# Kernel tuning notes

Measured on AMD Instinct MI355X. Metric: run time of the kernel, lower is better.

## Reference

```python
import jax, jax.numpy as jnp
import numpy as np

N_NODES = 50000
N_EDGES = 800000
D_IN = 128
D_OUT = 128


def setup_inputs() -> dict:
    key = jax.random.key(0)
    k1, k2, k3, k4 = jax.random.split(key, 4)
    node_features = jax.random.normal(k1, (N_NODES, D_IN), dtype=jnp.float32)
    edge_index = jax.random.randint(k2, (2, N_EDGES), 0, N_NODES, dtype=jnp.int64)
    # nn.Linear params: weight [out, in], bias [out]
    W = jax.random.normal(k3, (D_OUT, D_IN), dtype=jnp.float32) / np.sqrt(D_IN)
    b = jax.random.normal(k4, (D_OUT,), dtype=jnp.float32) * 0.01
    return {"node_features": node_features, "edge_index": edge_index, "W": W, "b": b}


def reference(node_features, edge_index, W, b):
    source_nodes = edge_index[0]
    dest_nodes = edge_index[1]
    # gather neighbor features [E, D_in], scatter-add into [N, D_in]
    neighbor_features = node_features[source_nodes]
    aggregated = jax.ops.segment_sum(neighbor_features, dest_nodes,
                                     num_segments=node_features.shape[0])
    # nn.Linear: x @ W.T + b
    return aggregated @ W.T + b
```

## Files before the change

kernel.cpp:

```cpp
#include <hip/hip_runtime.h>


constexpr int NN = 50000;
constexpr int NE = 800000;
constexpr int D  = 128;

constexpr int BS   = 128;
constexpr int NB   = (NN + BS - 1) / BS;
constexpr int EPB  = 4096;
constexpr int NSB  = (NE + EPB - 1) / EPB;
constexpr int CAP  = 4096;

constexpr int AROWU = 136;

typedef __attribute__((ext_vector_type(8))) short bf16x8;
typedef __attribute__((ext_vector_type(4))) float f32x4;

__device__ inline unsigned short f2bf(float f) {
    unsigned u = __float_as_uint(f);
    return (unsigned short)((u + 0x7fffu + ((u >> 16) & 1u)) >> 16);
}
__device__ inline float bflo(unsigned v) { return __uint_as_float(v << 16); }
__device__ inline float bfhi(unsigned v) { return __uint_as_float(v & 0xffff0000u); }

constexpr int NF4 = NN * D / 4;
constexpr int W4  = D * D / 4;
constexpr int NBLK_P = (NF4 + W4 + 511) / 512;
constexpr int GRID_A = NSB + NBLK_P;

__global__ __launch_bounds__(512) void k_prep_bucket(
    const float* __restrict__ nf, const float* __restrict__ W,
    const int* __restrict__ ei,
    ushort* __restrict__ nfh, ushort* __restrict__ Wh,
    ushort* __restrict__ offs, unsigned* __restrict__ buf)
{
    __shared__ int hist[NB], off[NB], cur[NB];
    __shared__ unsigned spk[EPB];
    const int t = threadIdx.x;

    if (blockIdx.x < NSB) {
        const int blk = blockIdx.x;
        const int e0  = blk * EPB;
        int cnt = NE - e0; if (cnt > EPB) cnt = EPB;

        for (int i = t; i < NB; i += 512) hist[i] = 0;
        __syncthreads();

        unsigned pk[8];
        #pragma unroll
        for (int j = 0; j < 8; ++j) {
            int idx = j * 512 + t;
            if (idx < cnt) {
                int e = e0 + idx;
                unsigned s = (unsigned)ei[e];
                unsigned d = (unsigned)ei[NE + e];
                pk[j] = (d << 16) | s;
                atomicAdd(&hist[pk[j] >> 23], 1);
            }
        }
        __syncthreads();
        if (t < NB) off[t] = hist[t];
        __syncthreads();
        for (int o = 1; o < NB; o <<= 1) {
            int v = (t >= o && t < NB) ? off[t - o] : 0;
            __syncthreads();
            if (t < NB) off[t] += v;
            __syncthreads();
        }
        if (t < NB) {
            int ex = off[t] - hist[t];
            cur[t] = ex;
            offs[blk * (NB + 1) + t] = (ushort)ex;
        }
        if (t == 0) offs[blk * (NB + 1) + NB] = (ushort)cnt;
        __syncthreads();
        #pragma unroll
        for (int j = 0; j < 8; ++j) {
            int idx = j * 512 + t;
            if (idx < cnt) {
                int l = atomicAdd(&cur[pk[j] >> 23], 1);
                spk[l] = pk[j];
            }
        }
        __syncthreads();
        for (int i = t; i < cnt; i += 512)
            buf[(size_t)blk * EPB + i] = spk[i];
    } else {
        int i = (blockIdx.x - NSB) * 512 + t;
        if (i < NF4) {
            float4 v = ((const float4*)nf)[i];
            ((ushort4*)nfh)[i] = make_ushort4(f2bf(v.x), f2bf(v.y), f2bf(v.z), f2bf(v.w));
        } else if (i < NF4 + W4) {
            int k = i - NF4;
            float4 v = ((const float4*)W)[k];
            ((ushort4*)Wh)[k] = make_ushort4(f2bf(v.x), f2bf(v.y), f2bf(v.z), f2bf(v.w));
        }
    }
}

__global__ __launch_bounds__(1024, 8) void k_sort_agg(
    const unsigned* __restrict__ nfh, const unsigned* __restrict__ buf,
    const ushort* __restrict__ offs, const ushort* __restrict__ Wh,
    const float* __restrict__ bias, float* __restrict__ out)
{
    __shared__ unsigned pkbuf[CAP];
    __shared__ ushort srt[CAP];
    __shared__ int scnt[256];
    __shared__ int sbase[NSB], rbase[NSB];
    __shared__ int hist[BS], off[BS], cur[BS];
    __shared__ __align__(16) unsigned tile[BS * AROWU / 2];
    const int b = blockIdx.x, t = threadIdx.x;
    const int lane = t & 63, w = t >> 6;

    int my = 0;
    if (t < NSB) {
        int o0 = (int)offs[t * (NB + 1) + b];
        int o1 = (int)offs[t * (NB + 1) + b + 1];
        rbase[t] = o0;
        my = o1 - o0;
    }
    if (t < 256) scnt[t] = (t < NSB) ? my : 0;
    if (t < BS) hist[t] = 0;
    __syncthreads();
    for (int o = 1; o < 256; o <<= 1) {
        int v = (t >= o && t < 256) ? scnt[t - o] : 0;
        __syncthreads();
        if (t < 256) scnt[t] += v;
        __syncthreads();
    }
    if (t < NSB) sbase[t] = scnt[t] - my;
    __syncthreads();
    int total = scnt[NSB - 1];
    if (total > CAP) total = CAP;

    for (int p = t; p < total; p += 1024) {
        int lo = 0, hi = NSB - 1;
        while (lo < hi) {
            int mid = (lo + hi) >> 1;
            if (scnt[mid] > p) hi = mid; else lo = mid + 1;
        }
        unsigned pk = buf[(size_t)lo * EPB + rbase[lo] + (p - sbase[lo])];
        pkbuf[p] = pk;
        atomicAdd(&hist[(pk >> 16) & (BS - 1)], 1);
    }
    __syncthreads();

    if (t < BS) off[t] = hist[t];
    __syncthreads();
    for (int o = 1; o < BS; o <<= 1) {
        int v = (t >= o && t < BS) ? off[t - o] : 0;
        __syncthreads();
        if (t < BS) off[t] += v;
        __syncthreads();
    }
    if (t < BS) { int ex = off[t] - hist[t]; off[t] = ex; cur[t] = ex; }
    __syncthreads();
    for (int e = t; e < total; e += 1024) {
        unsigned pk = pkbuf[e];
        int n = (pk >> 16) & (BS - 1);
        int p = atomicAdd(&cur[n], 1);
        srt[p] = (ushort)(pk & 0xffffu);
    }
    __syncthreads();

    const int qq = lane >> 4;
    const int sl = lane & 15;
    const uint4* nfv = (const uint4*)nfh;

    #pragma unroll 1
    for (int i = 0; i < 8; ++i) {
        const int n = w * 8 + i;
        const int beg = off[n], e = beg + hist[n];
        float accA[8] = {0,0,0,0,0,0,0,0};
        float accB[8] = {0,0,0,0,0,0,0,0};
        for (int p = beg; p < e; p += 16) {
            const int lim = e - 1;
            uint4 v[4];
            #pragma unroll
            for (int j = 0; j < 4; ++j) {
                int pos = p + 4 * j + qq;
                bool ok = pos <= lim;
                if (!ok) pos = lim;
                int s = srt[pos];
                uint4 val = nfv[(size_t)s * 16 + sl];
                v[j].x = ok ? val.x : 0u;
                v[j].y = ok ? val.y : 0u;
                v[j].z = ok ? val.z : 0u;
                v[j].w = ok ? val.w : 0u;
            }
            #pragma unroll
            for (int j = 0; j < 4; ++j) {
                float* A = (j & 1) ? accB : accA;
                A[0] += bflo(v[j].x); A[1] += bfhi(v[j].x);
                A[2] += bflo(v[j].y); A[3] += bfhi(v[j].y);
                A[4] += bflo(v[j].z); A[5] += bfhi(v[j].z);
                A[6] += bflo(v[j].w); A[7] += bfhi(v[j].w);
            }
        }
        float r[8];
        #pragma unroll
        for (int k = 0; k < 8; ++k) {
            float x = accA[k] + accB[k];
            x += __shfl_xor(x, 16);
            x += __shfl_xor(x, 32);
            r[k] = x;
        }
        if (qq == 0) {
            uint4 o;
            o.x = (unsigned)f2bf(r[0]) | ((unsigned)f2bf(r[1]) << 16);
            o.y = (unsigned)f2bf(r[2]) | ((unsigned)f2bf(r[3]) << 16);
            o.z = (unsigned)f2bf(r[4]) | ((unsigned)f2bf(r[5]) << 16);
            o.w = (unsigned)f2bf(r[6]) | ((unsigned)f2bf(r[7]) << 16);
            *(uint4*)(tile + n * (AROWU / 2) + sl * 4) = o;
        }
    }
    __syncthreads();

    const int m = lane & 15, q = lane >> 4;
    const ushort* lds = (const ushort*)tile;
    #pragma unroll
    for (int i = 0; i < 4; ++i) {
        const int task = w + 16 * i;
        const int t16  = task >> 3;
        const int c0   = (task & 7) * 16;
        const int grow0 = b * BS + t16 * 16;
        if (grow0 < NN) {
            bf16x8 a[4];
            const ushort* arow = lds + (t16 * 16 + m) * AROWU + q * 8;
            #pragma unroll
            for (int kk = 0; kk < 4; ++kk)
                a[kk] = *(const bf16x8*)(arow + kk * 32);
            float bv = bias[c0 + m];
            f32x4 acc = { bv, bv, bv, bv };
            const ushort* wrow = Wh + (size_t)(c0 + m) * D + q * 8;
            #pragma unroll
            for (int kk = 0; kk < 4; ++kk) {
                bf16x8 bb = *(const bf16x8*)(wrow + kk * 32);
                acc = __builtin_amdgcn_mfma_f32_16x16x32_bf16(a[kk], bb, acc, 0, 0, 0);
            }
            float* op = out + (size_t)(grow0 + q * 4) * D + c0 + m;
            op[0]     = acc[0];
            op[D]     = acc[1];
            op[2 * D] = acc[2];
            op[3 * D] = acc[3];
        }
    }
}

extern "C" void kernel_launch(void* const* d_in, const int* in_sizes, int n_in,
                              void* d_out, int out_size, void* d_ws, size_t ws_size,
                              hipStream_t stream) {
    const float* nf = (const float*)d_in[0];
    const int*   ei = (const int*)d_in[1];
    const float* W  = (const float*)d_in[2];
    const float* b  = (const float*)d_in[3];
    float* out = (float*)d_out;

    ushort*   nfh  = (ushort*)d_ws;
    ushort*   Wh   = nfh + (size_t)NN * D;
    unsigned* buf  = (unsigned*)(Wh + D * D);
    ushort*   offs = (ushort*)(buf + (size_t)NSB * EPB);

    k_prep_bucket<<<GRID_A, 512, 0, stream>>>(nf, W, ei, nfh, Wh, offs, buf);
    k_sort_agg   <<<NB, 1024, 0, stream>>>((const unsigned*)nfh, buf, offs, Wh, b, out);
}
```

Baseline: 133.6 us.

## Use wavefront scans, transpose offsets layout, and per-quarter-wave node aggregation

Replaces the barrier-heavy LDS Hillis-Steele prefix scans in both kernels with wavefront shuffle scans plus a small cross-wave fixup, which removes many __syncthreads. Stores the bucket offsets transposed so the aggregation kernel reads them coalesced. Keeps gathered edge keys in registers instead of an LDS staging buffer. The gather loop now gives each 16-lane quarter-wave its own destination node, which drops the cross-lane shuffle reduction but makes per-node work imbalanced across lanes in a wave.

```diff
diff --git a/kernel.cpp b/kernel.cpp
--- a/kernel.cpp
+++ b/kernel.cpp
@@ -15,6 +15,7 @@
 
 typedef __attribute__((ext_vector_type(8))) short bf16x8;
 typedef __attribute__((ext_vector_type(4))) float f32x4;
+typedef __attribute__((ext_vector_type(2))) float f32x2;
 
 __device__ inline unsigned short f2bf(float f) {
     unsigned u = __float_as_uint(f);
@@ -22,6 +23,22 @@
 }
 __device__ inline float bflo(unsigned v) { return __uint_as_float(v << 16); }
 __device__ inline float bfhi(unsigned v) { return __uint_as_float(v & 0xffff0000u); }
+
+__device__ inline int wscan(int v) {
+    #pragma unroll
+    for (int o = 1; o < 64; o <<= 1) {
+        int u = __shfl_up(v, o);
+        if ((int)(threadIdx.x & 63) >= o) v += u;
+    }
+    return v;
+}
+
+__device__ inline void acc8(f32x2& a0, f32x2& a1, f32x2& a2, f32x2& a3, uint4 v) {
+    a0 += (f32x2){bflo(v.x), bfhi(v.x)};
+    a1 += (f32x2){bflo(v.y), bfhi(v.y)};
+    a2 += (f32x2){bflo(v.z), bfhi(v.z)};
+    a3 += (f32x2){bflo(v.w), bfhi(v.w)};
+}
 
 constexpr int NF4 = NN * D / 4;
 constexpr int W4  = D * D / 4;
@@ -34,9 +51,10 @@
     ushort* __restrict__ nfh, ushort* __restrict__ Wh,
     ushort* __restrict__ offs, unsigned* __restrict__ buf)
 {
-    __shared__ int hist[NB], off[NB], cur[NB];
+    __shared__ int hist[NB], cur[NB];
+    __shared__ int wsum[8];
     __shared__ unsigned spk[EPB];
-    const int t = threadIdx.x;
+    const int t = threadIdx.x, lane = t & 63, w = t >> 6;
 
     if (blockIdx.x < NSB) {
         const int blk = blockIdx.x;
@@ -59,20 +77,20 @@
             }
         }
         __syncthreads();
-        if (t < NB) off[t] = hist[t];
-        __syncthreads();
-        for (int o = 1; o < NB; o <<= 1) {
-            int v = (t >= o && t < NB) ? off[t - o] : 0;
-            __syncthreads();
-            if (t < NB) off[t] += v;
-            __syncthreads();
-        }
+        int h = (t < NB) ? hist[t] : 0;
+        int v = wscan(h);
+        if (lane == 63) wsum[w] = v;
+        __syncthreads();
+        int addv = 0;
+        #pragma unroll
+        for (int i = 0; i < 8; ++i) addv += (i < w) ? wsum[i] : 0;
+        v += addv;
         if (t < NB) {
-            int ex = off[t] - hist[t];
+            int ex = v - h;
             cur[t] = ex;
-            offs[blk * (NB + 1) + t] = (ushort)ex;
-        }
-        if (t == 0) offs[blk * (NB + 1) + NB] = (ushort)cnt;
+            offs[t * NSB + blk] = (ushort)ex;
+        }
+        if (t == 0) offs[NB * NSB + blk] = (ushort)cnt;
         __syncthreads();
         #pragma unroll
         for (int j = 0; j < 8; ++j) {
@@ -103,63 +121,80 @@
     const ushort* __restrict__ offs, const ushort* __restrict__ Wh,
     const float* __restrict__ bias, float* __restrict__ out)
 {
-    __shared__ unsigned pkbuf[CAP];
     __shared__ ushort srt[CAP];
     __shared__ int scnt[256];
     __shared__ int sbase[NSB], rbase[NSB];
     __shared__ int hist[BS], off[BS], cur[BS];
+    __shared__ int wred[16];
     __shared__ __align__(16) unsigned tile[BS * AROWU / 2];
     const int b = blockIdx.x, t = threadIdx.x;
     const int lane = t & 63, w = t >> 6;
 
     int my = 0;
     if (t < NSB) {
-        int o0 = (int)offs[t * (NB + 1) + b];
-        int o1 = (int)offs[t * (NB + 1) + b + 1];
+        int o0 = (int)offs[b * NSB + t];
+        int o1 = (int)offs[(b + 1) * NSB + t];
         rbase[t] = o0;
         my = o1 - o0;
     }
-    if (t < 256) scnt[t] = (t < NSB) ? my : 0;
     if (t < BS) hist[t] = 0;
-    __syncthreads();
-    for (int o = 1; o < 256; o <<= 1) {
-        int v = (t >= o && t < 256) ? scnt[t - o] : 0;
-        __syncthreads();
-        if (t < 256) scnt[t] += v;
-        __syncthreads();
-    }
-    if (t < NSB) sbase[t] = scnt[t] - my;
+    int vs = 0;
+    if (w < 4) {
+        vs = wscan(my);
+        if (lane == 63) wred[w] = vs;
+    }
+    __syncthreads();
+    if (w < 4) {
+        int addv = 0;
+        #pragma unroll
+        for (int i = 0; i < 3; ++i) addv += (i < w) ? wred[i] : 0;
+        vs += addv;
+        scnt[t] = vs;
+        if (t < NSB) sbase[t] = vs - my;
+    }
     __syncthreads();
     int total = scnt[NSB - 1];
     if (total > CAP) total = CAP;
 
-    for (int p = t; p < total; p += 1024) {
-        int lo = 0, hi = NSB - 1;
-        while (lo < hi) {
-            int mid = (lo + hi) >> 1;
-            if (scnt[mid] > p) hi = mid; else lo = mid + 1;
-        }
-        unsigned pk = buf[(size_t)lo * EPB + rbase[lo] + (p - sbase[lo])];
-        pkbuf[p] = pk;
-        atomicAdd(&hist[(pk >> 16) & (BS - 1)], 1);
-    }
-    __syncthreads();
-
-    if (t < BS) off[t] = hist[t];
-    __syncthreads();
-    for (int o = 1; o < BS; o <<= 1) {
-        int v = (t >= o && t < BS) ? off[t - o] : 0;
-        __syncthreads();
-        if (t < BS) off[t] += v;
-        __syncthreads();
-    }
-    if (t < BS) { int ex = off[t] - hist[t]; off[t] = ex; cur[t] = ex; }
-    __syncthreads();
-    for (int e = t; e < total; e += 1024) {
-        unsigned pk = pkbuf[e];
-        int n = (pk >> 16) & (BS - 1);
-        int p = atomicAdd(&cur[n], 1);
-        srt[p] = (ushort)(pk & 0xffffu);
+    unsigned mypk[4];
+    int mycnt = 0;
+    #pragma unroll
+    for (int j = 0; j < 4; ++j) {
+        int p = t + j * 1024;
+        if (p < total) {
+            int lo = 0, hi = NSB - 1;
+            while (lo < hi) {
+                int mid = (lo + hi) >> 1;
+                if (scnt[mid] > p) hi = mid; else lo = mid + 1;
+            }
+            unsigned pk = buf[(size_t)lo * EPB + rbase[lo] + (p - sbase[lo])];
+            mypk[j] = pk;
+            atomicAdd(&hist[(pk >> 16) & (BS - 1)], 1);
+            mycnt = j + 1;
+        }
+    }
+    __syncthreads();
+
+    int hv = (t < BS) ? hist[t] : 0;
+    int nv = 0;
+    if (w < 2) {
+        nv = wscan(hv);
+        if (lane == 63) wred[8 + w] = nv;
+    }
+    __syncthreads();
+    if (t < BS) {
+        int ex = nv + ((w == 1) ? wred[8] : 0) - hv;
+        off[t] = ex; cur[t] = ex;
+    }
+    __syncthreads();
+    #pragma unroll
+    for (int j = 0; j < 4; ++j) {
+        if (j < mycnt) {
+            unsigned pk = mypk[j];
+            int n = (pk >> 16) & (BS - 1);
+            int p = atomicAdd(&cur[n], 1);
+            srt[p] = (ushort)(pk & 0xffffu);
+        }
     }
     __syncthreads();
 
@@ -168,51 +203,30 @@
     const uint4* nfv = (const uint4*)nfh;
 
     #pragma unroll 1
-    for (int i = 0; i < 8; ++i) {
-        const int n = w * 8 + i;
-        const int beg = off[n], e = beg + hist[n];
-        float accA[8] = {0,0,0,0,0,0,0,0};
-        float accB[8] = {0,0,0,0,0,0,0,0};
-        for (int p = beg; p < e; p += 16) {
-            const int lim = e - 1;
-            uint4 v[4];
-            #pragma unroll
-            for (int j = 0; j < 4; ++j) {
-                int pos = p + 4 * j + qq;
-                bool ok = pos <= lim;
-                if (!ok) pos = lim;
-                int s = srt[pos];
-                uint4 val = nfv[(size_t)s * 16 + sl];
-                v[j].x = ok ? val.x : 0u;
-                v[j].y = ok ? val.y : 0u;
-                v[j].z = ok ? val.z : 0u;
-                v[j].w = ok ? val.w : 0u;
-            }
-            #pragma unroll
-            for (int j = 0; j < 4; ++j) {
-                float* A = (j & 1) ? accB : accA;
-                A[0] += bflo(v[j].x); A[1] += bfhi(v[j].x);
-                A[2] += bflo(v[j].y); A[3] += bfhi(v[j].y);
-                A[4] += bflo(v[j].z); A[5] += bfhi(v[j].z);
-                A[6] += bflo(v[j].w); A[7] += bfhi(v[j].w);
-            }
-        }
-        float r[8];
-        #pragma unroll
-        for (int k = 0; k < 8; ++k) {
-            float x = accA[k] + accB[k];
-            x += __shfl_xor(x, 16);
-            x += __shfl_xor(x, 32);
-            r[k] = x;
-        }
-        if (qq == 0) {
-            uint4 o;
-            o.x = (unsigned)f2bf(r[0]) | ((unsigned)f2bf(r[1]) << 16);
-            o.y = (unsigned)f2bf(r[2]) | ((unsigned)f2bf(r[3]) << 16);
-            o.z = (unsigned)f2bf(r[4]) | ((unsigned)f2bf(r[5]) << 16);
-            o.w = (unsigned)f2bf(r[6]) | ((unsigned)f2bf(r[7]) << 16);
-            *(uint4*)(tile + n * (AROWU / 2) + sl * 4) = o;
-        }
+    for (int i = 0; i < 2; ++i) {
+        const int n = w * 8 + i * 4 + qq;
+        const int beg = off[n], cnt = hist[n];
+        f32x2 a0 = {0.f, 0.f}, a1 = {0.f, 0.f}, a2 = {0.f, 0.f}, a3 = {0.f, 0.f};
+        int p = 0;
+        for (; p + 2 <= cnt; p += 2) {
+            const int s0 = srt[beg + p];
+            const int s1 = srt[beg + p + 1];
+            const uint4 v0 = nfv[(size_t)s0 * 16 + sl];
+            const uint4 v1 = nfv[(size_t)s1 * 16 + sl];
+            acc8(a0, a1, a2, a3, v0);
+            acc8(a0, a1, a2, a3, v1);
+        }
+        if (p < cnt) {
+            const int s0 = srt[beg + p];
+            const uint4 v0 = nfv[(size_t)s0 * 16 + sl];
+            acc8(a0, a1, a2, a3, v0);
+        }
+        uint4 o;
+        o.x = (unsigned)f2bf(a0.x) | ((unsigned)f2bf(a0.y) << 16);
+        o.y = (unsigned)f2bf(a1.x) | ((unsigned)f2bf(a1.y) << 16);
+        o.z = (unsigned)f2bf(a2.x) | ((unsigned)f2bf(a2.y) << 16);
+        o.w = (unsigned)f2bf(a3.x) | ((unsigned)f2bf(a3.y) << 16);
+        *(uint4*)(tile + n * (AROWU / 2) + sl * 4) = o;
     }
     __syncthreads();
 
```

Measured after the change: 128.3 us. -4.0%, faster.
